# Kernel optimization log

Hardware: AMD Instinct MI355X
Metric: run time of the kernel (lower is better)

The kernel has to match this reference:

```python
import jax, jax.numpy as jnp
import numpy as np

B, S, D_MODEL, N_HEADS, HEAD_DIM = 4, 2048, 1024, 16, 64
NEG = -1e9


def apply_rope_real(x, cos_f, sin_f):
    # x: [B, H, S, D]; cos_f/sin_f: [S, D//2] broadcast over B, H
    x_even = x[..., ::2]
    x_odd = x[..., 1::2]
    out_even = x_even * cos_f - x_odd * sin_f
    out_odd = x_even * sin_f + x_odd * cos_f
    return jnp.stack([out_even, out_odd], axis=-1).reshape(x.shape)


def setup_inputs() -> dict:
    key = jax.random.key(0)
    ks = jax.random.split(key, 8)
    x = jax.random.normal(ks[0], (B, S, D_MODEL), dtype=jnp.float32)
    # RoPE tables: theta_i = 10000^{-2i/d}, angles = pos * theta
    inv_freq = 1.0 / (10000.0 ** (jnp.arange(0, HEAD_DIM, 2, dtype=jnp.float32) / HEAD_DIM))
    angles = jnp.arange(S, dtype=jnp.float32)[:, None] * inv_freq[None, :]  # [S, D/2]
    cos_freqs = jnp.cos(angles)
    sin_freqs = jnp.sin(angles)
    causal_mask = jnp.where(jnp.tril(jnp.ones((S, S), dtype=bool)), 0.0, NEG).astype(jnp.float32)
    scale = 0.02
    w_q = jax.random.normal(ks[1], (D_MODEL, D_MODEL), dtype=jnp.float32) * scale
    w_k = jax.random.normal(ks[2], (D_MODEL, D_MODEL), dtype=jnp.float32) * scale
    w_v = jax.random.normal(ks[3], (D_MODEL, D_MODEL), dtype=jnp.float32) * scale
    w_o = jax.random.normal(ks[4], (D_MODEL, D_MODEL), dtype=jnp.float32) * scale
    return {"x": x, "cos_freqs": cos_freqs, "sin_freqs": sin_freqs,
            "causal_mask": causal_mask, "w_q": w_q, "w_k": w_k, "w_v": w_v, "w_o": w_o}


def reference(x, cos_freqs, sin_freqs, causal_mask, w_q, w_k, w_v, w_o):
    batch, seq_len, _ = x.shape
    scale = 1.0 / jnp.sqrt(jnp.float32(HEAD_DIM))
    # torch Linear: y = x @ W.T
    def proj(w):
        return (x @ w.T).reshape(batch, seq_len, N_HEADS, HEAD_DIM).transpose(0, 2, 1, 3)
    q = apply_rope_real(proj(w_q), cos_freqs, sin_freqs)
    k = apply_rope_real(proj(w_k), cos_freqs, sin_freqs)
    v = proj(w_v)
    attn = jnp.einsum('bhqd,bhkd->bhqk', q, k) * scale + causal_mask
    attn = jax.nn.softmax(attn, axis=-1)
    out = jnp.einsum('bhqk,bhkd->bhqd', attn, v)
    out = out.transpose(0, 2, 1, 3).reshape(batch, seq_len, -1)
    return out @ w_o.T
```

## Files before the change

kernel.cpp:

```cpp
#include <hip/hip_runtime.h>
#include <stdint.h>

#define B_  4
#define S_  2048
#define DM_ 1024
#define NH_ 16
#define HD_ 64

typedef unsigned short ushort_t;
typedef __bf16 bf16x8 __attribute__((ext_vector_type(8)));
typedef float  floatx4 __attribute__((ext_vector_type(4)));
typedef float  floatx16 __attribute__((ext_vector_type(16)));

__device__ __forceinline__ float bf2f(ushort_t u) {
    union { unsigned int i; float f; } v; v.i = ((unsigned int)u) << 16; return v.f;
}
__device__ __forceinline__ ushort_t f2bf(float f) {
    union { float f; unsigned int i; } v; v.f = f;
    unsigned int x = v.i;
    return (ushort_t)((x + 0x7fffu + ((x >> 16) & 1u)) >> 16);
}
__device__ __forceinline__ unsigned int pack_bf16_trunc(float lo, float hi) {
    union { float f; unsigned int u; } a, b;
    a.f = lo; b.f = hi;
    return __builtin_amdgcn_perm(b.u, a.u, 0x07060302u);
}

#define QSCALE 0.1803368801f

__global__ __launch_bounds__(256) void cvt_all_kernel(
    const float* __restrict__ x,  const float* __restrict__ wq,
    const float* __restrict__ wk, const float* __restrict__ wv,
    const float* __restrict__ wo,
    ushort_t* __restrict__ xb,  ushort_t* __restrict__ wqb,
    ushort_t* __restrict__ wkb, ushort_t* __restrict__ wvb,
    ushort_t* __restrict__ wob)
{
    const int blk = blockIdx.x;
    const float* src; ushort_t* dst; int off;
    if (blk < 8192)       { src = x;  dst = xb;  off = blk; }
    else if (blk < 9216)  { src = wq; dst = wqb; off = blk - 8192; }
    else if (blk < 10240) { src = wk; dst = wkb; off = blk - 9216; }
    else if (blk < 11264) { src = wv; dst = wvb; off = blk - 10240; }
    else                  { src = wo; dst = wob; off = blk - 11264; }
    const int i = off * 256 + threadIdx.x;
    float4 v = ((const float4*)src)[i];
    ushort4 o; o.x = f2bf(v.x); o.y = f2bf(v.y); o.z = f2bf(v.z); o.w = f2bf(v.w);
    ((ushort4*)dst)[i] = o;
}

__global__ __launch_bounds__(512, 1) void gemm_qkv_kernel(
    const ushort_t* __restrict__ A,
    const ushort_t* __restrict__ B0, const ushort_t* __restrict__ B1,
    const ushort_t* __restrict__ B2,
    void* __restrict__ C0, void* __restrict__ C1, void* __restrict__ C2,
    const float* __restrict__ cf, const float* __restrict__ sf,
    int M, int N, int K, int nz)
{
    __shared__ ushort_t As[2][16384];
    __shared__ ushort_t Bs[2][8192];

    const int lid = blockIdx.x;
    const int cpx = gridDim.x >> 3;
    const int wg  = (lid & 7) * cpx + (lid >> 3);
    const int x   = wg / (8 * nz);
    const int rr  = wg - x * (8 * nz);
    const int y   = rr & 7;
    const int z   = rr >> 3;

    const ushort_t* Bw = z == 0 ? B0 : z == 1 ? B1 : B2;
    void* Cv           = z == 0 ? C0 : z == 1 ? C1 : C2;

    const int tid  = threadIdx.x;
    const int wave = tid >> 6, lane = tid & 63;
    const int l15 = lane & 15, quad = lane >> 4;
    const int wr = wave >> 1, wc = wave & 1;
    const int mbase = x * 256;
    const int nbase = y * 128;
    const int NT = K >> 6;

    auto stageA = [&](int bt, int t) {
#pragma unroll
        for (int L = 0; L < 4; ++L) {
            const int e8  = L * 512 + tid;
            const int row = e8 >> 3, c = e8 & 7;
            const ushort_t* src = A + (size_t)(mbase + row) * K + t * 64 + ((c ^ (row & 7)) << 3);
            __builtin_amdgcn_global_load_lds(
                (const __attribute__((address_space(1))) unsigned int*)src,
                (__attribute__((address_space(3))) unsigned int*)(&As[bt][e8 * 8]), 16, 0, 0);
        }
    };
    auto stageB = [&](int bt, int t) {
#pragma unroll
        for (int L = 0; L < 2; ++L) {
            const int e8  = L * 512 + tid;
            const int row = e8 >> 3, c = e8 & 7;
            const ushort_t* src = Bw + (size_t)(nbase + row) * K + t * 64 + ((c ^ (row & 7)) << 3);
            __builtin_amdgcn_global_load_lds(
                (const __attribute__((address_space(1))) unsigned int*)src,
                (__attribute__((address_space(3))) unsigned int*)(&Bs[bt][e8 * 8]), 16, 0, 0);
        }
    };

    floatx4 acc[4][4] = {};

    stageA(0, 0);
    stageB(0, 0);
    if (NT > 1) {
        stageB(1, 1);
        asm volatile("s_waitcnt vmcnt(2)" ::: "memory");
    } else {
        asm volatile("s_waitcnt vmcnt(0)" ::: "memory");
    }
    __builtin_amdgcn_s_barrier();

    for (int t = 0; t < NT; ++t) {
        const int bt = t & 1;
        bf16x8 af[2][4], bf[2][4];

#pragma unroll
        for (int kk = 0; kk < 2; ++kk) {
#pragma unroll
            for (int f = 0; f < 4; ++f) {
                const int row = wr * 64 + f * 16 + l15;
                af[kk][f] = *(const bf16x8*)&As[bt][row * 64 + ((((kk << 2) | quad)) ^ (l15 & 7)) * 8];
            }
#pragma unroll
            for (int g = 0; g < 4; ++g) {
                const int row = wc * 64 + g * 16 + l15;
                bf[kk][g] = *(const bf16x8*)&Bs[bt][row * 64 + ((((kk << 2) | quad)) ^ (l15 & 7)) * 8];
            }
        }
        if (t + 1 < NT) stageA(bt ^ 1, t + 1);
        asm volatile("s_waitcnt lgkmcnt(0)" ::: "memory");
        __builtin_amdgcn_s_barrier();
        __builtin_amdgcn_s_setprio(1);
#pragma unroll
        for (int kk = 0; kk < 2; ++kk)
#pragma unroll
            for (int mt = 0; mt < 2; ++mt)
#pragma unroll
                for (int nt = 0; nt < 4; ++nt)
                    acc[mt][nt] = __builtin_amdgcn_mfma_f32_16x16x32_bf16(
                        af[kk][mt], bf[kk][nt], acc[mt][nt], 0, 0, 0);
        __builtin_amdgcn_s_setprio(0);

        if (t + 2 < NT) stageB(bt, t + 2);
        __builtin_amdgcn_s_setprio(1);
#pragma unroll
        for (int kk = 0; kk < 2; ++kk)
#pragma unroll
            for (int mt = 0; mt < 2; ++mt)
#pragma unroll
                for (int nt = 0; nt < 4; ++nt)
                    acc[2 + mt][nt] = __builtin_amdgcn_mfma_f32_16x16x32_bf16(
                        af[kk][2 + mt], bf[kk][nt], acc[2 + mt][nt], 0, 0, 0);
        __builtin_amdgcn_s_setprio(0);
        if (t + 2 < NT) { asm volatile("s_waitcnt vmcnt(2)" ::: "memory"); }
        else            { asm volatile("s_waitcnt vmcnt(0)" ::: "memory"); }
        __builtin_amdgcn_s_barrier();
    }

    const float qs = (z == 0) ? QSCALE : 1.0f;
#pragma unroll
    for (int mt = 0; mt < 4; ++mt) {
#pragma unroll
        for (int nt = 0; nt < 4; ++nt) {
            const int col = nbase + wc * 64 + nt * 16 + l15;
            const int m0  = mbase + wr * 64 + mt * 16 + quad * 4;
            if (z == 2) {
                const int b = m0 >> 11, s = m0 & 2047;
                const int hh = col >> 6, d = col & 63;
                uint2 pk;
                pk.x = (unsigned)f2bf(acc[mt][nt][0]) | ((unsigned)f2bf(acc[mt][nt][1]) << 16);
                pk.y = (unsigned)f2bf(acc[mt][nt][2]) | ((unsigned)f2bf(acc[mt][nt][3]) << 16);
                *(uint2*)&((ushort_t*)Cv)[((size_t)((b * NH_ + hh) * HD_ + d)) * S_ + s] = pk;
            } else {
                const int d = col & 63, j = d >> 1;
                const int hh = col >> 6;
                const float sgn = (l15 & 1) ? 1.0f : -1.0f;
#pragma unroll
                for (int r = 0; r < 4; ++r) {
                    const int m = m0 + r;
                    const int b = m >> 11, s = m & 2047;
                    const float v = acc[mt][nt][r];
                    const float p = __shfl_xor(v, 1, 64);
                    const float c  = cf[s * 32 + j] * qs;
                    const float sn = sf[s * 32 + j] * qs * sgn;
                    ((ushort_t*)Cv)[(((size_t)(b * NH_ + hh)) * S_ + s) * HD_ + d] =
                        f2bf(v * c + p * sn);
                }
            }
        }
    }
}

__global__ __launch_bounds__(256, 2) void gemm_proj_kernel(
    const ushort_t* __restrict__ A, const ushort_t* __restrict__ Bw,
    float* __restrict__ Cv, int M, int N, int K)
{
    __shared__ ushort_t As[2][8192];
    __shared__ ushort_t Bs[2][8192];

    const int lid = blockIdx.x;
    const int cpx = gridDim.x >> 3;
    const int wg  = (lid & 7) * cpx + (lid >> 3);
    const int x   = wg >> 3;
    const int y   = wg & 7;

    const int tid  = threadIdx.x;
    const int wave = tid >> 6, lane = tid & 63;
    const int l15 = lane & 15, quad = lane >> 4;
    const int wr = wave >> 1, wc = wave & 1;
    const int mbase = x * 128;
    const int nbase = y * 128;
    const int NT = K >> 6;

    auto stageA = [&](int bt, int t) {
#pragma unroll
        for (int L = 0; L < 4; ++L) {
            const int e   = L * 256 + tid;
            const int row = e >> 3, c = e & 7;
            const ushort_t* src = A + (size_t)(mbase + row) * K + t * 64 + ((c ^ (row & 7)) << 3);
            __builtin_amdgcn_global_load_lds(
                (const __attribute__((address_space(1))) unsigned int*)src,
                (__attribute__((address_space(3))) unsigned int*)(&As[bt][e * 8]), 16, 0, 0);
        }
    };
    auto stageB = [&](int bt, int t) {
#pragma unroll
        for (int L = 0; L < 4; ++L) {
            const int e   = L * 256 + tid;
            const int row = e >> 3, c = e & 7;
            const ushort_t* src = Bw + (size_t)(nbase + row) * K + t * 64 + ((c ^ (row & 7)) << 3);
            __builtin_amdgcn_global_load_lds(
                (const __attribute__((address_space(1))) unsigned int*)src,
                (__attribute__((address_space(3))) unsigned int*)(&Bs[bt][e * 8]), 16, 0, 0);
        }
    };

    floatx4 acc[4][4] = {};

    stageA(0, 0);
    stageB(0, 0);
    if (NT > 1) {
        stageB(1, 1);
        asm volatile("s_waitcnt vmcnt(4)" ::: "memory");
    } else {
        asm volatile("s_waitcnt vmcnt(0)" ::: "memory");
    }
    __builtin_amdgcn_s_barrier();

    for (int t = 0; t < NT; ++t) {
        const int bt = t & 1;
        bf16x8 a0[2][2], a1[2][2], bf[2][4];

#pragma unroll
        for (int kk = 0; kk < 2; ++kk) {
#pragma unroll
            for (int f = 0; f < 2; ++f) {
                const int row = wr * 64 + f * 16 + l15;
                a0[kk][f] = *(const bf16x8*)&As[bt][row * 64 + ((((kk << 2) | quad)) ^ (l15 & 7)) * 8];
            }
#pragma unroll
            for (int g = 0; g < 4; ++g) {
                const int row = wc * 64 + g * 16 + l15;
                bf[kk][g] = *(const bf16x8*)&Bs[bt][row * 64 + ((((kk << 2) | quad)) ^ (l15 & 7)) * 8];
            }
        }
        if (t + 1 < NT) stageA(bt ^ 1, t + 1);
        asm volatile("s_waitcnt lgkmcnt(8)" ::: "memory");
        __builtin_amdgcn_s_barrier();
        asm volatile("s_waitcnt lgkmcnt(0)" ::: "memory");
        __builtin_amdgcn_s_setprio(1);
#pragma unroll
        for (int kk = 0; kk < 2; ++kk)
#pragma unroll
            for (int mt = 0; mt < 2; ++mt)
#pragma unroll
                for (int nt = 0; nt < 4; ++nt)
                    acc[mt][nt] = __builtin_amdgcn_mfma_f32_16x16x32_bf16(
                        a0[kk][mt], bf[kk][nt], acc[mt][nt], 0, 0, 0);
        __builtin_amdgcn_s_setprio(0);
        __builtin_amdgcn_s_barrier();

#pragma unroll
        for (int kk = 0; kk < 2; ++kk)
#pragma unroll
            for (int f = 0; f < 2; ++f) {
                const int row = wr * 64 + 32 + f * 16 + l15;
                a1[kk][f] = *(const bf16x8*)&As[bt][row * 64 + ((((kk << 2) | quad)) ^ (l15 & 7)) * 8];
            }
        if (t + 2 < NT) stageB(bt, t + 2);
        __builtin_amdgcn_s_barrier();
        asm volatile("s_waitcnt lgkmcnt(0)" ::: "memory");
        __builtin_amdgcn_s_setprio(1);
#pragma unroll
        for (int kk = 0; kk < 2; ++kk)
#pragma unroll
            for (int mt = 0; mt < 2; ++mt)
#pragma unroll
                for (int nt = 0; nt < 4; ++nt)
                    acc[2 + mt][nt] = __builtin_amdgcn_mfma_f32_16x16x32_bf16(
                        a1[kk][mt], bf[kk][nt], acc[2 + mt][nt], 0, 0, 0);
        __builtin_amdgcn_s_setprio(0);
        if (t + 2 < NT) { asm volatile("s_waitcnt vmcnt(4)" ::: "memory"); }
        else            { asm volatile("s_waitcnt vmcnt(0)" ::: "memory"); }
        __builtin_amdgcn_s_barrier();
    }

#pragma unroll
    for (int mt = 0; mt < 4; ++mt) {
#pragma unroll
        for (int nt = 0; nt < 4; ++nt) {
            const int col = nbase + wc * 64 + nt * 16 + l15;
            const int m0  = mbase + wr * 64 + mt * 16 + quad * 4;
#pragma unroll
            for (int r = 0; r < 4; ++r)
                Cv[(size_t)(m0 + r) * N + col] = acc[mt][nt][r];
        }
    }
}

__global__ __launch_bounds__(256, 4) void attn_kernel(
    const ushort_t* __restrict__ Qg, const ushort_t* __restrict__ Kg,
    const ushort_t* __restrict__ Vg, ushort_t* __restrict__ Og)
{
    __shared__ ushort_t Ks[2][64 * 64];
    __shared__ ushort_t Vt[2][64 * 64];

    const int qt_tab[16] = {15,13,11,9, 0,2,4,6, 14,12,10,8, 1,3,5,7};

    const int id   = blockIdx.x;
    const int sg   = id >> 3;
    const int bh   = (id & 7) * 8 + (sg & 7);
    const int qtile = qt_tab[sg >> 3];
    const int tid  = threadIdx.x;
    const int wave = tid >> 6, lane = tid & 63;
    const int l31 = lane & 31, h = lane >> 5;

    const size_t bh_off = (size_t)bh * S_ * HD_;
    const int b_out = bh >> 4, h_out = bh & 15;

    const int e0 = tid, e1 = tid + 256;
    const int r0 = e0 >> 3, c0 = (e0 & 7) ^ (r0 & 7);
    const int r1 = e1 >> 3, c1 = (e1 & 7) ^ (r1 & 7);

    const int qbase = qtile * 128;
    const int nkt   = 2 * qtile + 2;
    const int qrow  = qbase + wave * 32 + l31;

    bf16x8 qf[4];
#pragma unroll
    for (int ks = 0; ks < 4; ++ks)
        qf[ks] = *(const bf16x8*)(Qg + bh_off + (size_t)qrow * HD_ + ks * 16 + h * 8);

    float m_run = -1e30f, l_run = 0.f;
    floatx16 o_acc[2] = {};

    {
        const ushort_t* ka = Kg + bh_off + (size_t)r0 * HD_ + c0 * 8;
        const ushort_t* kb = Kg + bh_off + (size_t)r1 * HD_ + c1 * 8;
        const ushort_t* va = Vg + bh_off + (size_t)r0 * S_ + c0 * 8;
        const ushort_t* vb = Vg + bh_off + (size_t)r1 * S_ + c1 * 8;
        __builtin_amdgcn_global_load_lds(
            (const __attribute__((address_space(1))) unsigned int*)ka,
            (__attribute__((address_space(3))) unsigned int*)(&Ks[0][e0 * 8]), 16, 0, 0);
        __builtin_amdgcn_global_load_lds(
            (const __attribute__((address_space(1))) unsigned int*)kb,
            (__attribute__((address_space(3))) unsigned int*)(&Ks[0][e1 * 8]), 16, 0, 0);
        __builtin_amdgcn_global_load_lds(
            (const __attribute__((address_space(1))) unsigned int*)va,
            (__attribute__((address_space(3))) unsigned int*)(&Vt[0][e0 * 8]), 16, 0, 0);
        __builtin_amdgcn_global_load_lds(
            (const __attribute__((address_space(1))) unsigned int*)vb,
            (__attribute__((address_space(3))) unsigned int*)(&Vt[0][e1 * 8]), 16, 0, 0);
    }
    asm volatile("s_waitcnt vmcnt(0)" ::: "memory");
    __syncthreads();

    for (int kt = 0; kt < nkt; ++kt) {
        const int kbase = kt * 64;
        const int cur = kt & 1;

        if (kt + 1 < nkt) {
            const int nb = kbase + 64;
            const ushort_t* ka = Kg + bh_off + (size_t)(nb + r0) * HD_ + c0 * 8;
            const ushort_t* kb = Kg + bh_off + (size_t)(nb + r1) * HD_ + c1 * 8;
            const ushort_t* va = Vg + bh_off + (size_t)r0 * S_ + nb + c0 * 8;
            const ushort_t* vb = Vg + bh_off + (size_t)r1 * S_ + nb + c1 * 8;
            __builtin_amdgcn_global_load_lds(
                (const __attribute__((address_space(1))) unsigned int*)ka,
                (__attribute__((address_space(3))) unsigned int*)(&Ks[cur ^ 1][e0 * 8]), 16, 0, 0);
            __builtin_amdgcn_global_load_lds(
                (const __attribute__((address_space(1))) unsigned int*)kb,
                (__attribute__((address_space(3))) unsigned int*)(&Ks[cur ^ 1][e1 * 8]), 16, 0, 0);
            __builtin_amdgcn_global_load_lds(
                (const __attribute__((address_space(1))) unsigned int*)va,
                (__attribute__((address_space(3))) unsigned int*)(&Vt[cur ^ 1][e0 * 8]), 16, 0, 0);
            __builtin_amdgcn_global_load_lds(
                (const __attribute__((address_space(1))) unsigned int*)vb,
                (__attribute__((address_space(3))) unsigned int*)(&Vt[cur ^ 1][e1 * 8]), 16, 0, 0);
        }

        if (kbase <= qbase + wave * 32 + 31) {
            floatx16 st[2] = {};
#pragma unroll
            for (int nt = 0; nt < 2; ++nt) {
                const int krow = nt * 32 + l31;
#pragma unroll
                for (int ks = 0; ks < 4; ++ks) {
                    bf16x8 kf = *(const bf16x8*)&Ks[cur][krow * 64 +
                                    (((ks * 2 + h) ^ (l31 & 7)) << 3)];
                    st[nt] = __builtin_amdgcn_mfma_f32_32x32x16_bf16(kf, qf[ks], st[nt], 0, 0, 0);
                }
            }
            if (kbase + 63 > qbase + wave * 32) {
#pragma unroll
                for (int nt = 0; nt < 2; ++nt) {
                    const int key0 = kbase + nt * 32 + 4 * h;
#pragma unroll
                    for (int c = 0; c < 4; ++c)
#pragma unroll
                        for (int r = 0; r < 4; ++r)
                            if (key0 + 8 * c + r > qrow) st[nt][c * 4 + r] = -1e9f;
                }
            }
            float mx = st[0][0];
#pragma unroll
            for (int nt = 0; nt < 2; ++nt)
#pragma unroll
                for (int i = 0; i < 16; ++i) mx = fmaxf(mx, st[nt][i]);
            mx = fmaxf(mx, __shfl_xor(mx, 32, 64));
            if (!__all(mx <= m_run + 8.0f)) {
                const float mnew = fmaxf(m_run, mx);
                const float alpha = __builtin_amdgcn_exp2f(m_run - mnew);
                m_run = mnew;
                l_run *= alpha;
#pragma unroll
                for (int dt = 0; dt < 2; ++dt)
#pragma unroll
                    for (int i = 0; i < 16; ++i) o_acc[dt][i] *= alpha;
            }
            float sum = 0.f;
#pragma unroll
            for (int nt = 0; nt < 2; ++nt)
#pragma unroll
                for (int i = 0; i < 16; ++i) {
                    const float p = __builtin_amdgcn_exp2f(st[nt][i] - m_run);
                    st[nt][i] = p; sum += p;
                }
            sum += __shfl_xor(sum, 32, 64);
            l_run += sum;

            bf16x8 pf[4];
#pragma unroll
            for (int ks = 0; ks < 4; ++ks) {
                const int nt = ks >> 1, base = (ks & 1) * 8;
                unsigned wrd[4];
#pragma unroll
                for (int d8 = 0; d8 < 2; ++d8) {
                    unsigned p = pack_bf16_trunc(st[nt][base + 2 * d8],
                                                 st[nt][base + 2 * d8 + 1]);
                    unsigned q = pack_bf16_trunc(st[nt][base + 4 + 2 * d8],
                                                 st[nt][base + 4 + 2 * d8 + 1]);
                    auto r = __builtin_amdgcn_permlane32_swap((int)p, (int)q, false, false);
                    wrd[d8]     = (unsigned)r[0];
                    wrd[2 + d8] = (unsigned)r[1];
                }
                union { unsigned u[4]; bf16x8 v; } cvt;
                cvt.u[0] = wrd[0]; cvt.u[1] = wrd[1];
                cvt.u[2] = wrd[2]; cvt.u[3] = wrd[3];
                pf[ks] = cvt.v;
            }

#pragma unroll
            for (int dt = 0; dt < 2; ++dt) {
                const int d = dt * 32 + l31;
#pragma unroll
                for (int ks = 0; ks < 4; ++ks) {
                    bf16x8 vf = *(const bf16x8*)&Vt[cur][d * 64 +
                                    (((ks * 2 + h) ^ (l31 & 7)) << 3)];
                    o_acc[dt] = __builtin_amdgcn_mfma_f32_32x32x16_bf16(vf, pf[ks], o_acc[dt], 0, 0, 0);
                }
            }
        }

        asm volatile("s_waitcnt vmcnt(0)" ::: "memory");
        __syncthreads();
    }

    const float inv = 1.0f / l_run;
    ushort_t* orow = Og + ((size_t)(b_out * S_ + qrow)) * DM_ + h_out * HD_;
#pragma unroll
    for (int dt = 0; dt < 2; ++dt)
#pragma unroll
        for (int c = 0; c < 4; ++c) {
            uint2 pk;
            pk.x = (unsigned)f2bf(o_acc[dt][c * 4 + 0] * inv) |
                   ((unsigned)f2bf(o_acc[dt][c * 4 + 1] * inv) << 16);
            pk.y = (unsigned)f2bf(o_acc[dt][c * 4 + 2] * inv) |
                   ((unsigned)f2bf(o_acc[dt][c * 4 + 3] * inv) << 16);
            *(uint2*)(orow + dt * 32 + 8 * c + 4 * h) = pk;
        }
}

extern "C" void kernel_launch(void* const* d_in, const int* in_sizes, int n_in,
                              void* d_out, int out_size, void* d_ws, size_t ws_size,
                              hipStream_t stream)
{
    const float* x  = (const float*)d_in[0];
    const float* cf = (const float*)d_in[1];
    const float* sf = (const float*)d_in[2];
    const float* wq = (const float*)d_in[4];
    const float* wk = (const float*)d_in[5];
    const float* wv = (const float*)d_in[6];
    const float* wo = (const float*)d_in[7];
    float* out = (float*)d_out;

    const size_t NELEM = (size_t)B_ * S_ * DM_;
    const size_t WELEM = (size_t)DM_ * DM_;
    ushort_t* xb  = (ushort_t*)d_ws;
    ushort_t* qb  = xb + NELEM;
    ushort_t* kb  = qb + NELEM;
    ushort_t* vb  = kb + NELEM;
    ushort_t* ao  = vb + NELEM;
    ushort_t* wqb = ao + NELEM;
    ushort_t* wkb = wqb + WELEM;
    ushort_t* wvb = wkb + WELEM;
    ushort_t* wob = wvb + WELEM;

    cvt_all_kernel<<<dim3(8192 + 4 * 1024), 256, 0, stream>>>(
        x, wq, wk, wv, wo, xb, wqb, wkb, wvb, wob);

    const int M = B_ * S_;
    gemm_qkv_kernel<<<dim3(32 * 8 * 3), 512, 0, stream>>>(
        xb, wqb, wkb, wvb, qb, kb, vb, cf, sf, M, DM_, DM_, 3);
    attn_kernel<<<dim3(1024), 256, 0, stream>>>(qb, kb, vb, ao);
    gemm_proj_kernel<<<dim3(64 * 8), 256, 0, stream>>>(
        ao, wob, out, M, DM_, DM_);
}
```

Measured before the change: 253.9 us.

## Double attention query tile to 256 rows with 512-thread blocks

```diff
diff --git a/kernel.cpp b/kernel.cpp
--- a/kernel.cpp
+++ b/kernel.cpp
@@ -322,19 +322,17 @@
     }
 }
 
-__global__ __launch_bounds__(256, 4) void attn_kernel(
+__global__ __launch_bounds__(512, 2) void attn_kernel(
     const ushort_t* __restrict__ Qg, const ushort_t* __restrict__ Kg,
     const ushort_t* __restrict__ Vg, ushort_t* __restrict__ Og)
 {
     __shared__ ushort_t Ks[2][64 * 64];
     __shared__ ushort_t Vt[2][64 * 64];
 
-    const int qt_tab[16] = {15,13,11,9, 0,2,4,6, 14,12,10,8, 1,3,5,7};
-
     const int id   = blockIdx.x;
-    const int sg   = id >> 3;
-    const int bh   = (id & 7) * 8 + (sg & 7);
-    const int qtile = qt_tab[sg >> 3];
+    const int bh   = (id & 7) * 8 + ((id >> 3) & 7);
+    const int slot = id >> 6;
+    const int q    = slot < 4 ? 7 - slot : slot - 4;
     const int tid  = threadIdx.x;
     const int wave = tid >> 6, lane = tid & 63;
     const int l31 = lane & 31, h = lane >> 5;
@@ -342,12 +340,11 @@
     const size_t bh_off = (size_t)bh * S_ * HD_;
     const int b_out = bh >> 4, h_out = bh & 15;
 
-    const int e0 = tid, e1 = tid + 256;
-    const int r0 = e0 >> 3, c0 = (e0 & 7) ^ (r0 & 7);
-    const int r1 = e1 >> 3, c1 = (e1 & 7) ^ (r1 & 7);
-
-    const int qbase = qtile * 128;
-    const int nkt   = 2 * qtile + 2;
+    const int r0 = tid >> 3;
+    const int c0 = (tid & 7) ^ (r0 & 7);
+
+    const int qbase = q * 256;
+    const int nkt   = 4 * q + 4;
     const int qrow  = qbase + wave * 32 + l31;
 
     bf16x8 qf[4];
@@ -360,21 +357,13 @@
 
     {
         const ushort_t* ka = Kg + bh_off + (size_t)r0 * HD_ + c0 * 8;
-        const ushort_t* kb = Kg + bh_off + (size_t)r1 * HD_ + c1 * 8;
         const ushort_t* va = Vg + bh_off + (size_t)r0 * S_ + c0 * 8;
-        const ushort_t* vb = Vg + bh_off + (size_t)r1 * S_ + c1 * 8;
         __builtin_amdgcn_global_load_lds(
             (const __attribute__((address_space(1))) unsigned int*)ka,
-            (__attribute__((address_space(3))) unsigned int*)(&Ks[0][e0 * 8]), 16, 0, 0);
-        __builtin_amdgcn_global_load_lds(
-            (const __attribute__((address_space(1))) unsigned int*)kb,
-            (__attribute__((address_space(3))) unsigned int*)(&Ks[0][e1 * 8]), 16, 0, 0);
+            (__attribute__((address_space(3))) unsigned int*)(&Ks[0][tid * 8]), 16, 0, 0);
         __builtin_amdgcn_global_load_lds(
             (const __attribute__((address_space(1))) unsigned int*)va,
-            (__attribute__((address_space(3))) unsigned int*)(&Vt[0][e0 * 8]), 16, 0, 0);
-        __builtin_amdgcn_global_load_lds(
-            (const __attribute__((address_space(1))) unsigned int*)vb,
-            (__attribute__((address_space(3))) unsigned int*)(&Vt[0][e1 * 8]), 16, 0, 0);
+            (__attribute__((address_space(3))) unsigned int*)(&Vt[0][tid * 8]), 16, 0, 0);
     }
     asm volatile("s_waitcnt vmcnt(0)" ::: "memory");
     __syncthreads();
@@ -386,21 +375,13 @@
         if (kt + 1 < nkt) {
             const int nb = kbase + 64;
             const ushort_t* ka = Kg + bh_off + (size_t)(nb + r0) * HD_ + c0 * 8;
-            const ushort_t* kb = Kg + bh_off + (size_t)(nb + r1) * HD_ + c1 * 8;
             const ushort_t* va = Vg + bh_off + (size_t)r0 * S_ + nb + c0 * 8;
-            const ushort_t* vb = Vg + bh_off + (size_t)r1 * S_ + nb + c1 * 8;
             __builtin_amdgcn_global_load_lds(
                 (const __attribute__((address_space(1))) unsigned int*)ka,
-                (__attribute__((address_space(3))) unsigned int*)(&Ks[cur ^ 1][e0 * 8]), 16, 0, 0);
-            __builtin_amdgcn_global_load_lds(
-                (const __attribute__((address_space(1))) unsigned int*)kb,
-                (__attribute__((address_space(3))) unsigned int*)(&Ks[cur ^ 1][e1 * 8]), 16, 0, 0);
+                (__attribute__((address_space(3))) unsigned int*)(&Ks[cur ^ 1][tid * 8]), 16, 0, 0);
             __builtin_amdgcn_global_load_lds(
                 (const __attribute__((address_space(1))) unsigned int*)va,
-                (__attribute__((address_space(3))) unsigned int*)(&Vt[cur ^ 1][e0 * 8]), 16, 0, 0);
-            __builtin_amdgcn_global_load_lds(
-                (const __attribute__((address_space(1))) unsigned int*)vb,
-                (__attribute__((address_space(3))) unsigned int*)(&Vt[cur ^ 1][e1 * 8]), 16, 0, 0);
+                (__attribute__((address_space(3))) unsigned int*)(&Vt[cur ^ 1][tid * 8]), 16, 0, 0);
         }
 
         if (kbase <= qbase + wave * 32 + 31) {
@@ -462,9 +443,9 @@
                 for (int d8 = 0; d8 < 2; ++d8) {
                     unsigned p = pack_bf16_trunc(st[nt][base + 2 * d8],
                                                  st[nt][base + 2 * d8 + 1]);
-                    unsigned q = pack_bf16_trunc(st[nt][base + 4 + 2 * d8],
-                                                 st[nt][base + 4 + 2 * d8 + 1]);
-                    auto r = __builtin_amdgcn_permlane32_swap((int)p, (int)q, false, false);
+                    unsigned qv = pack_bf16_trunc(st[nt][base + 4 + 2 * d8],
+                                                  st[nt][base + 4 + 2 * d8 + 1]);
+                    auto r = __builtin_amdgcn_permlane32_swap((int)p, (int)qv, false, false);
                     wrd[d8]     = (unsigned)r[0];
                     wrd[2 + d8] = (unsigned)r[1];
                 }
@@ -536,7 +517,7 @@
     const int M = B_ * S_;
     gemm_qkv_kernel<<<dim3(32 * 8 * 3), 512, 0, stream>>>(
         xb, wqb, wkb, wvb, qb, kb, vb, cf, sf, M, DM_, DM_, 3);
-    attn_kernel<<<dim3(1024), 256, 0, stream>>>(qb, kb, vb, ao);
+    attn_kernel<<<dim3(512), 512, 0, stream>>>(qb, kb, vb, ao);
     gemm_proj_kernel<<<dim3(64 * 8), 256, 0, stream>>>(
         ao, wob, out, M, DM_, DM_);
 }
```

Result: slower. 264.1 us (+4.0%).

## Enlarge output-projection GEMM tile to 256x128 with 512 threads, drop mid-loop barriers

Applied to the files above, without the earlier changes.

```diff
diff --git a/kernel.cpp b/kernel.cpp
--- a/kernel.cpp
+++ b/kernel.cpp
@@ -195,11 +195,11 @@
     }
 }
 
-__global__ __launch_bounds__(256, 2) void gemm_proj_kernel(
+__global__ __launch_bounds__(512, 1) void gemm_proj_kernel(
     const ushort_t* __restrict__ A, const ushort_t* __restrict__ Bw,
     float* __restrict__ Cv, int M, int N, int K)
 {
-    __shared__ ushort_t As[2][8192];
+    __shared__ ushort_t As[2][16384];
     __shared__ ushort_t Bs[2][8192];
 
     const int lid = blockIdx.x;
@@ -212,30 +212,30 @@
     const int wave = tid >> 6, lane = tid & 63;
     const int l15 = lane & 15, quad = lane >> 4;
     const int wr = wave >> 1, wc = wave & 1;
-    const int mbase = x * 128;
+    const int mbase = x * 256;
     const int nbase = y * 128;
     const int NT = K >> 6;
 
     auto stageA = [&](int bt, int t) {
 #pragma unroll
         for (int L = 0; L < 4; ++L) {
-            const int e   = L * 256 + tid;
-            const int row = e >> 3, c = e & 7;
+            const int e8  = L * 512 + tid;
+            const int row = e8 >> 3, c = e8 & 7;
             const ushort_t* src = A + (size_t)(mbase + row) * K + t * 64 + ((c ^ (row & 7)) << 3);
             __builtin_amdgcn_global_load_lds(
                 (const __attribute__((address_space(1))) unsigned int*)src,
-                (__attribute__((address_space(3))) unsigned int*)(&As[bt][e * 8]), 16, 0, 0);
+                (__attribute__((address_space(3))) unsigned int*)(&As[bt][e8 * 8]), 16, 0, 0);
         }
     };
     auto stageB = [&](int bt, int t) {
 #pragma unroll
-        for (int L = 0; L < 4; ++L) {
-            const int e   = L * 256 + tid;
-            const int row = e >> 3, c = e & 7;
+        for (int L = 0; L < 2; ++L) {
+            const int e8  = L * 512 + tid;
+            const int row = e8 >> 3, c = e8 & 7;
             const ushort_t* src = Bw + (size_t)(nbase + row) * K + t * 64 + ((c ^ (row & 7)) << 3);
             __builtin_amdgcn_global_load_lds(
                 (const __attribute__((address_space(1))) unsigned int*)src,
-                (__attribute__((address_space(3))) unsigned int*)(&Bs[bt][e * 8]), 16, 0, 0);
+                (__attribute__((address_space(3))) unsigned int*)(&Bs[bt][e8 * 8]), 16, 0, 0);
         }
     };
 
@@ -245,7 +245,7 @@
     stageB(0, 0);
     if (NT > 1) {
         stageB(1, 1);
-        asm volatile("s_waitcnt vmcnt(4)" ::: "memory");
+        asm volatile("s_waitcnt vmcnt(2)" ::: "memory");
     } else {
         asm volatile("s_waitcnt vmcnt(0)" ::: "memory");
     }
@@ -253,14 +253,14 @@
 
     for (int t = 0; t < NT; ++t) {
         const int bt = t & 1;
-        bf16x8 a0[2][2], a1[2][2], bf[2][4];
+        bf16x8 af[2][4], bf[2][4];
 
 #pragma unroll
         for (int kk = 0; kk < 2; ++kk) {
 #pragma unroll
-            for (int f = 0; f < 2; ++f) {
+            for (int f = 0; f < 4; ++f) {
                 const int row = wr * 64 + f * 16 + l15;
-                a0[kk][f] = *(const bf16x8*)&As[bt][row * 64 + ((((kk << 2) | quad)) ^ (l15 & 7)) * 8];
+                af[kk][f] = *(const bf16x8*)&As[bt][row * 64 + ((((kk << 2) | quad)) ^ (l15 & 7)) * 8];
             }
 #pragma unroll
             for (int g = 0; g < 4; ++g) {
@@ -269,9 +269,8 @@
             }
         }
         if (t + 1 < NT) stageA(bt ^ 1, t + 1);
-        asm volatile("s_waitcnt lgkmcnt(8)" ::: "memory");
+        asm volatile("s_waitcnt lgkmcnt(0)" ::: "memory");
         __builtin_amdgcn_s_barrier();
-        asm volatile("s_waitcnt lgkmcnt(0)" ::: "memory");
         __builtin_amdgcn_s_setprio(1);
 #pragma unroll
         for (int kk = 0; kk < 2; ++kk)
@@ -280,20 +279,10 @@
 #pragma unroll
                 for (int nt = 0; nt < 4; ++nt)
                     acc[mt][nt] = __builtin_amdgcn_mfma_f32_16x16x32_bf16(
-                        a0[kk][mt], bf[kk][nt], acc[mt][nt], 0, 0, 0);
+                        af[kk][mt], bf[kk][nt], acc[mt][nt], 0, 0, 0);
         __builtin_amdgcn_s_setprio(0);
-        __builtin_amdgcn_s_barrier();
-
-#pragma unroll
-        for (int kk = 0; kk < 2; ++kk)
-#pragma unroll
-            for (int f = 0; f < 2; ++f) {
-                const int row = wr * 64 + 32 + f * 16 + l15;
-                a1[kk][f] = *(const bf16x8*)&As[bt][row * 64 + ((((kk << 2) | quad)) ^ (l15 & 7)) * 8];
-            }
+
         if (t + 2 < NT) stageB(bt, t + 2);
-        __builtin_amdgcn_s_barrier();
-        asm volatile("s_waitcnt lgkmcnt(0)" ::: "memory");
         __builtin_amdgcn_s_setprio(1);
 #pragma unroll
         for (int kk = 0; kk < 2; ++kk)
@@ -302,9 +291,9 @@
 #pragma unroll
                 for (int nt = 0; nt < 4; ++nt)
                     acc[2 + mt][nt] = __builtin_amdgcn_mfma_f32_16x16x32_bf16(
-                        a1[kk][mt], bf[kk][nt], acc[2 + mt][nt], 0, 0, 0);
+                        af[kk][2 + mt], bf[kk][nt], acc[2 + mt][nt], 0, 0, 0);
         __builtin_amdgcn_s_setprio(0);
-        if (t + 2 < NT) { asm volatile("s_waitcnt vmcnt(4)" ::: "memory"); }
+        if (t + 2 < NT) { asm volatile("s_waitcnt vmcnt(2)" ::: "memory"); }
         else            { asm volatile("s_waitcnt vmcnt(0)" ::: "memory"); }
         __builtin_amdgcn_s_barrier();
     }
@@ -537,6 +526,6 @@
     gemm_qkv_kernel<<<dim3(32 * 8 * 3), 512, 0, stream>>>(
         xb, wqb, wkb, wvb, qb, kb, vb, cf, sf, M, DM_, DM_, 3);
     attn_kernel<<<dim3(1024), 256, 0, stream>>>(qb, kb, vb, ao);
-    gemm_proj_kernel<<<dim3(64 * 8), 256, 0, stream>>>(
+    gemm_proj_kernel<<<dim3(32 * 8), 512, 0, stream>>>(
         ao, wob, out, M, DM_, DM_);
 }
```

Measured after the change: 255.0 us. About the same (+0.4%).

## Halve QKV GEMM K-tile to 32 and raise occupancy to four blocks per CU

Applied to the files above, without the earlier changes.

```diff
diff --git a/kernel.cpp b/kernel.cpp
--- a/kernel.cpp
+++ b/kernel.cpp
@@ -49,7 +49,7 @@
     ((ushort4*)dst)[i] = o;
 }
 
-__global__ __launch_bounds__(512, 1) void gemm_qkv_kernel(
+__global__ __launch_bounds__(512, 4) void gemm_qkv_kernel(
     const ushort_t* __restrict__ A,
     const ushort_t* __restrict__ B0, const ushort_t* __restrict__ B1,
     const ushort_t* __restrict__ B2,
@@ -57,8 +57,8 @@
     const float* __restrict__ cf, const float* __restrict__ sf,
     int M, int N, int K, int nz)
 {
-    __shared__ ushort_t As[2][16384];
-    __shared__ ushort_t Bs[2][8192];
+    __shared__ ushort_t As[2][8192];
+    __shared__ ushort_t Bs[2][4096];
 
     const int lid = blockIdx.x;
     const int cpx = gridDim.x >> 3;
@@ -77,29 +77,27 @@
     const int wr = wave >> 1, wc = wave & 1;
     const int mbase = x * 256;
     const int nbase = y * 128;
-    const int NT = K >> 6;
+    const int NT = K >> 5;
 
     auto stageA = [&](int bt, int t) {
 #pragma unroll
-        for (int L = 0; L < 4; ++L) {
-            const int e8  = L * 512 + tid;
-            const int row = e8 >> 3, c = e8 & 7;
-            const ushort_t* src = A + (size_t)(mbase + row) * K + t * 64 + ((c ^ (row & 7)) << 3);
+        for (int L = 0; L < 2; ++L) {
+            const int e   = L * 512 + tid;
+            const int row = e >> 2, c = e & 3;
+            const ushort_t* src = A + (size_t)(mbase + row) * K + t * 32 +
+                                  ((c ^ ((row >> 1) & 3)) << 3);
             __builtin_amdgcn_global_load_lds(
                 (const __attribute__((address_space(1))) unsigned int*)src,
-                (__attribute__((address_space(3))) unsigned int*)(&As[bt][e8 * 8]), 16, 0, 0);
+                (__attribute__((address_space(3))) unsigned int*)(&As[bt][e * 8]), 16, 0, 0);
         }
     };
     auto stageB = [&](int bt, int t) {
-#pragma unroll
-        for (int L = 0; L < 2; ++L) {
-            const int e8  = L * 512 + tid;
-            const int row = e8 >> 3, c = e8 & 7;
-            const ushort_t* src = Bw + (size_t)(nbase + row) * K + t * 64 + ((c ^ (row & 7)) << 3);
-            __builtin_amdgcn_global_load_lds(
-                (const __attribute__((address_space(1))) unsigned int*)src,
-                (__attribute__((address_space(3))) unsigned int*)(&Bs[bt][e8 * 8]), 16, 0, 0);
-        }
+        const int row = tid >> 2, c = tid & 3;
+        const ushort_t* src = Bw + (size_t)(nbase + row) * K + t * 32 +
+                              ((c ^ ((row >> 1) & 3)) << 3);
+        __builtin_amdgcn_global_load_lds(
+            (const __attribute__((address_space(1))) unsigned int*)src,
+            (__attribute__((address_space(3))) unsigned int*)(&Bs[bt][tid * 8]), 16, 0, 0);
     };
 
     floatx4 acc[4][4] = {};
@@ -108,7 +106,7 @@
     stageB(0, 0);
     if (NT > 1) {
         stageB(1, 1);
-        asm volatile("s_waitcnt vmcnt(2)" ::: "memory");
+        asm volatile("s_waitcnt vmcnt(1)" ::: "memory");
     } else {
         asm volatile("s_waitcnt vmcnt(0)" ::: "memory");
     }
@@ -116,47 +114,40 @@
 
     for (int t = 0; t < NT; ++t) {
         const int bt = t & 1;
-        bf16x8 af[2][4], bf[2][4];
-
-#pragma unroll
-        for (int kk = 0; kk < 2; ++kk) {
-#pragma unroll
-            for (int f = 0; f < 4; ++f) {
-                const int row = wr * 64 + f * 16 + l15;
-                af[kk][f] = *(const bf16x8*)&As[bt][row * 64 + ((((kk << 2) | quad)) ^ (l15 & 7)) * 8];
-            }
-#pragma unroll
-            for (int g = 0; g < 4; ++g) {
-                const int row = wc * 64 + g * 16 + l15;
-                bf[kk][g] = *(const bf16x8*)&Bs[bt][row * 64 + ((((kk << 2) | quad)) ^ (l15 & 7)) * 8];
-            }
+        bf16x8 af[4], bf[4];
+
+#pragma unroll
+        for (int f = 0; f < 4; ++f) {
+            const int row = wr * 64 + f * 16 + l15;
+            af[f] = *(const bf16x8*)&As[bt][row * 32 + ((quad ^ ((row >> 1) & 3)) << 3)];
+        }
+#pragma unroll
+        for (int g = 0; g < 4; ++g) {
+            const int row = wc * 64 + g * 16 + l15;
+            bf[g] = *(const bf16x8*)&Bs[bt][row * 32 + ((quad ^ ((row >> 1) & 3)) << 3)];
         }
         if (t + 1 < NT) stageA(bt ^ 1, t + 1);
         asm volatile("s_waitcnt lgkmcnt(0)" ::: "memory");
         __builtin_amdgcn_s_barrier();
         __builtin_amdgcn_s_setprio(1);
 #pragma unroll
-        for (int kk = 0; kk < 2; ++kk)
-#pragma unroll
-            for (int mt = 0; mt < 2; ++mt)
-#pragma unroll
-                for (int nt = 0; nt < 4; ++nt)
-                    acc[mt][nt] = __builtin_amdgcn_mfma_f32_16x16x32_bf16(
-                        af[kk][mt], bf[kk][nt], acc[mt][nt], 0, 0, 0);
+        for (int mt = 0; mt < 2; ++mt)
+#pragma unroll
+            for (int nt = 0; nt < 4; ++nt)
+                acc[mt][nt] = __builtin_amdgcn_mfma_f32_16x16x32_bf16(
+                    af[mt], bf[nt], acc[mt][nt], 0, 0, 0);
         __builtin_amdgcn_s_setprio(0);
 
         if (t + 2 < NT) stageB(bt, t + 2);
         __builtin_amdgcn_s_setprio(1);
 #pragma unroll
-        for (int kk = 0; kk < 2; ++kk)
-#pragma unroll
-            for (int mt = 0; mt < 2; ++mt)
-#pragma unroll
-                for (int nt = 0; nt < 4; ++nt)
-                    acc[2 + mt][nt] = __builtin_amdgcn_mfma_f32_16x16x32_bf16(
-                        af[kk][2 + mt], bf[kk][nt], acc[2 + mt][nt], 0, 0, 0);
+        for (int mt = 0; mt < 2; ++mt)
+#pragma unroll
+            for (int nt = 0; nt < 4; ++nt)
+                acc[2 + mt][nt] = __builtin_amdgcn_mfma_f32_16x16x32_bf16(
+                    af[2 + mt], bf[nt], acc[2 + mt][nt], 0, 0, 0);
         __builtin_amdgcn_s_setprio(0);
-        if (t + 2 < NT) { asm volatile("s_waitcnt vmcnt(2)" ::: "memory"); }
+        if (t + 2 < NT) { asm volatile("s_waitcnt vmcnt(1)" ::: "memory"); }
         else            { asm volatile("s_waitcnt vmcnt(0)" ::: "memory"); }
         __builtin_amdgcn_s_barrier();
     }
```

Result: no change. 255.0 us (+0.5%).
